# Optimization experiments

Hardware: AMD Instinct MI355X
Metric: run time of the kernel (lower is better)

The kernel has to match this reference:

```python
import jax, jax.numpy as jnp
import numpy as np

B, T, N, D = 4, 12, 512, 128
L = 4            # max_lag + 1 lag encoders
H = D // 2       # lag-encoder hidden dim
THRESHOLD = 0.1


def setup_inputs() -> dict:
    key = jax.random.key(0)
    ks = jax.random.split(key, 10)
    s = 0.02
    return {
        "x":   jax.random.normal(ks[0], (B, T, N, D), dtype=jnp.float32),
        # lag encoders: Linear(D->H), ReLU, Linear(H->D), stacked over L lags
        "W1":  s * jax.random.normal(ks[1], (L, D, H), dtype=jnp.float32),
        "b1":  jnp.zeros((L, H), dtype=jnp.float32),
        "W2":  s * jax.random.normal(ks[2], (L, H, D), dtype=jnp.float32),
        "b2":  jnp.zeros((L, D), dtype=jnp.float32),
        # causal scorer: Linear(2D->D), ReLU, (Dropout=id in eval), Linear(D->1), Sigmoid
        "Ws1": s * jax.random.normal(ks[3], (2 * D, D), dtype=jnp.float32),
        "bs1": jnp.zeros((D,), dtype=jnp.float32),
        "Ws2": s * jax.random.normal(ks[4], (D, 1), dtype=jnp.float32),
        "bs2": jnp.zeros((1,), dtype=jnp.float32),
    }


def reference(x, W1, b1, W2, b2, Ws1, bs1, Ws2, bs2):
    Tdim = x.shape[1]
    # lagged slices x[:, T-1-lag] for lag in 0..L-1 (all lags active since T > max_lag)
    lags = jnp.stack([x[:, max(0, Tdim - 1 - l)] for l in range(L)], axis=1)  # (B,L,N,D)
    h = jax.nn.relu(jnp.einsum('blnd,ldh->blnh', lags, W1) + b1[None, :, None, :])
    enc = jnp.einsum('blnh,lhd->blnd', h, W2) + b2[None, :, None, :]          # (B,L,N,D)
    agg = enc.mean(axis=1)                                                    # (B,N,D)

    # pairwise causal scorer. cat([src, tgt]) @ Ws1 == src @ Ws1[:D] + tgt @ Ws1[D:],
    # avoiding the explicit (B,N,N,2D) concat.
    src_proj = jnp.einsum('bnd,dk->bnk', agg, Ws1[:D])   # (B,N,D)
    tgt_proj = jnp.einsum('bnd,dk->bnk', agg, Ws1[D:])   # (B,N,D)
    pre = src_proj[:, :, None, :] + tgt_proj[:, None, :, :] + bs1  # (B,N,N,D)
    score = jax.nn.sigmoid(jnp.einsum('bijd,d->bij', jax.nn.relu(pre), Ws2[:, 0]) + bs2[0])

    # threshold sparsification + remove self loops
    adj = jnp.where(score > THRESHOLD, score, 0.0)
    adj = adj * (1.0 - jnp.eye(N, dtype=adj.dtype))

    # multi-hop propagation and global max normalization per batch element
    a2 = jnp.matmul(adj, adj)
    a3 = jnp.matmul(a2, adj)
    enhanced = adj + 0.5 * a2 + 0.25 * a3
    mx = jnp.max(enhanced, axis=(-1, -2), keepdims=True)
    return enhanced / (mx + 1e-8)
```

## Files before the change

### kernel.cpp

```cpp
#include <hip/hip_runtime.h>
#include <math.h>

#define Bn 4
#define Tn 12
#define Nn 512
#define Dn 128
#define Ln 4
#define Hn 64

typedef __attribute__((ext_vector_type(8))) short short8;
typedef __attribute__((ext_vector_type(4))) float f32x4;
typedef _Float16 h2 __attribute__((ext_vector_type(2)));

__device__ __forceinline__ unsigned short f2bf(float f) {
    unsigned int u = __float_as_uint(f);
    unsigned int r = (u + 0x7FFF + ((u >> 16) & 1)) >> 16;
    return (unsigned short)r;
}
__device__ __forceinline__ float bf2f(unsigned short s) {
    return __uint_as_float(((unsigned int)s) << 16);
}
__device__ __forceinline__ float fdot2(h2 a, h2 b, float c) {
#if defined(__has_builtin)
#if __has_builtin(__builtin_amdgcn_fdot2)
    return __builtin_amdgcn_fdot2(a, b, c, false);
#else
    return c + (float)a.x*(float)b.x + (float)a.y*(float)b.y;
#endif
#else
    return c + (float)a.x*(float)b.x + (float)a.y*(float)b.y;
#endif
}

__global__ __launch_bounds__(256) void k_prep(
    const float* __restrict__ W1, const float* __restrict__ W2, const float* __restrict__ Ws1,
    unsigned short* __restrict__ w1p, unsigned short* __restrict__ w2p,
    unsigned short* __restrict__ wsp)
{
    int g = blockIdx.x*256 + threadIdx.x;
    unsigned short tmp[8];
    if (g < 4096) {
        int lag = g >> 10, r = g & 1023;
        int n = r >> 4, k8 = r & 15;
        #pragma unroll
        for (int j = 0; j < 8; ++j) tmp[j] = f2bf(W1[(size_t)(lag*128 + k8*8 + j)*64 + n]);
        *(short8*)(w1p + (size_t)lag*8192 + n*128 + k8*8) = *(const short8*)tmp;
    } else if (g < 8192) {
        int r = g - 4096;
        int n = r >> 5, k8 = r & 31;
        #pragma unroll
        for (int j = 0; j < 8; ++j) tmp[j] = f2bf(W2[(size_t)(k8*8 + j)*128 + n]);
        *(short8*)(w2p + (size_t)n*256 + k8*8) = *(const short8*)tmp;
    } else {
        int r = g - 8192;
        int tgt = r >> 11, r2 = r & 2047;
        int n = r2 >> 4, k8 = r2 & 15;
        #pragma unroll
        for (int j = 0; j < 8; ++j) tmp[j] = f2bf(Ws1[(size_t)(tgt*128 + k8*8 + j)*128 + n]);
        *(short8*)(wsp + (size_t)tgt*16384 + n*128 + k8*8) = *(const short8*)tmp;
    }
}

__global__ __launch_bounds__(256) void k_enc(
    const float* __restrict__ x,  const float* __restrict__ b1,
    const float* __restrict__ b2, const float* __restrict__ bs1,
    const unsigned short* __restrict__ w1p, const unsigned short* __restrict__ w2p,
    const unsigned short* __restrict__ wsp,
    unsigned short* __restrict__ spb, unsigned short* __restrict__ tpb,
    unsigned int* __restrict__ maxslot)
{
    __shared__ __align__(16) unsigned short hA[16*264];
    __shared__ __align__(16) unsigned short xA[16*136];
    __shared__ __align__(16) unsigned short aggA[16*136];
    int tid  = threadIdx.x;
    int bid  = blockIdx.x;
    int wv   = __builtin_amdgcn_readfirstlane(tid >> 6);
    int lane = tid & 63;
    if (bid == 0 && tid < Bn) maxslot[tid] = 0u;

    int r0 = bid * 16;
    int bb = r0 >> 9, n0 = r0 & 511;
    int m = lane & 15, q = lane >> 4;
    int colL = lane & 15, rq = lane >> 4;

    for (int lag = 0; lag < Ln; ++lag) {
        __syncthreads();
        {
            const float4* xs = (const float4*)(x + ((size_t)(bb*Tn + (Tn-1-lag))*Nn + n0)*Dn);
            for (int v = tid; v < 512; v += 256) {
                float4 f = xs[v];
                int row = v >> 5, c4 = v & 31;
                ushort4 o = { f2bf(f.x), f2bf(f.y), f2bf(f.z), f2bf(f.w) };
                *(ushort4*)&xA[row*136 + c4*4] = o;
            }
        }
        __syncthreads();
        f32x4 acc = {0.f,0.f,0.f,0.f};
        #pragma unroll
        for (int ks = 0; ks < 4; ++ks) {
            short8 af = *(const short8*)&xA[m*136 + ks*32 + q*8];
            short8 bg = *(const short8*)(w1p + (size_t)lag*8192 + (wv*16+m)*128 + ks*32 + q*8);
            acc = __builtin_amdgcn_mfma_f32_16x16x32_bf16(af, bg, acc, 0, 0, 0);
        }
        int ncol = wv*16 + colL;
        float bv = b1[lag*Hn + ncol];
        #pragma unroll
        for (int reg = 0; reg < 4; ++reg)
            hA[(rq*4+reg)*264 + lag*64 + ncol] = f2bf(fmaxf(acc[reg] + bv, 0.f));
    }
    __syncthreads();

    #pragma unroll
    for (int ch = 0; ch < 2; ++ch) {
        f32x4 acc = {0.f,0.f,0.f,0.f};
        #pragma unroll
        for (int ks = 0; ks < 8; ++ks) {
            short8 af = *(const short8*)&hA[m*264 + ks*32 + q*8];
            short8 bg = *(const short8*)(w2p + (size_t)(ch*64 + wv*16 + m)*256 + ks*32 + q*8);
            acc = __builtin_amdgcn_mfma_f32_16x16x32_bf16(af, bg, acc, 0, 0, 0);
        }
        int col = ch*64 + wv*16 + colL;
        float b2s = b2[col] + b2[Dn+col] + b2[2*Dn+col] + b2[3*Dn+col];
        #pragma unroll
        for (int reg = 0; reg < 4; ++reg)
            aggA[(rq*4+reg)*136 + col] = f2bf(0.25f*(acc[reg] + b2s));
    }
    __syncthreads();

    #pragma unroll
    for (int tgt = 0; tgt < 2; ++tgt) {
        f32x4 acc[2] = {{0.f,0.f,0.f,0.f},{0.f,0.f,0.f,0.f}};
        #pragma unroll
        for (int ks = 0; ks < 4; ++ks) {
            short8 af = *(const short8*)&aggA[m*136 + ks*32 + q*8];
            #pragma unroll
            for (int nt = 0; nt < 2; ++nt) {
                short8 bg = *(const short8*)(wsp + (size_t)tgt*16384 + (wv*32 + nt*16 + m)*128 + ks*32 + q*8);
                acc[nt] = __builtin_amdgcn_mfma_f32_16x16x32_bf16(af, bg, acc[nt], 0, 0, 0);
            }
        }
        unsigned short* dst = tgt ? tpb : spb;
        #pragma unroll
        for (int nt = 0; nt < 2; ++nt) {
            int n = wv*32 + nt*16 + colL;
            float bv = tgt ? 0.f : bs1[n];
            #pragma unroll
            for (int reg = 0; reg < 4; ++reg) {
                _Float16 hv = (_Float16)(acc[nt][reg] + bv);
                dst[(size_t)(r0 + rq*4 + reg)*Dn + n] = __builtin_bit_cast(unsigned short, hv);
            }
        }
    }
}

__global__ __launch_bounds__(256) void k_score(
    const unsigned short* __restrict__ spb, const unsigned short* __restrict__ tpb,
    const float* __restrict__ Ws2, const float* __restrict__ bs2,
    unsigned short* __restrict__ adj_b, unsigned short* __restrict__ adj_bt)
{
    __shared__ unsigned int spl[64*65];
    __shared__ unsigned int tpl[64*65];
    __shared__ unsigned int wl[64];
    int tid = threadIdx.x;
    int wv = __builtin_amdgcn_readfirstlane(tid >> 6);
    int lane = tid & 63;
    int bz = blockIdx.z;
    int i0b = blockIdx.y * 64, j0b = blockIdx.x * 64;
    const unsigned short* spr = spb + (size_t)bz*Nn*Dn;
    const unsigned short* tpr = tpb + (size_t)bz*Nn*Dn;

    for (int v = tid; v < 1024; v += 256) {
        int row = v >> 4, c = v & 15;
        uint4 gs = *(const uint4*)(spr + (size_t)(i0b+row)*Dn + c*8);
        uint4 gt = *(const uint4*)(tpr + (size_t)(j0b+row)*Dn + c*8);
        spl[row*65 + c*4 + 0] = gs.x; spl[row*65 + c*4 + 1] = gs.y;
        spl[row*65 + c*4 + 2] = gs.z; spl[row*65 + c*4 + 3] = gs.w;
        tpl[row*65 + c*4 + 0] = gt.x; tpl[row*65 + c*4 + 1] = gt.y;
        tpl[row*65 + c*4 + 2] = gt.z; tpl[row*65 + c*4 + 3] = gt.w;
    }
    if (tid < 64) {
        h2 hw = { (_Float16)Ws2[tid*2], (_Float16)Ws2[tid*2+1] };
        wl[tid] = __builtin_bit_cast(unsigned int, hw);
    }
    __syncthreads();

    int iq = lane >> 4, jq = lane & 15;
    int iw = wv*16 + iq*4;
    float acc[4][4] = {};
    #pragma unroll 4
    for (int c = 0; c < 64; ++c) {
        h2 wp = __builtin_bit_cast(h2, wl[c]);
        h2 sh[4], th[4];
        #pragma unroll
        for (int ii = 0; ii < 4; ++ii) sh[ii] = __builtin_bit_cast(h2, spl[(iw+ii)*65 + c]);
        #pragma unroll
        for (int jj = 0; jj < 4; ++jj) th[jj] = __builtin_bit_cast(h2, tpl[(jq*4+jj)*65 + c]);
        #pragma unroll
        for (int ii = 0; ii < 4; ++ii)
            #pragma unroll
            for (int jj = 0; jj < 4; ++jj) {
                h2 r = __builtin_elementwise_max(sh[ii] + th[jj], (h2){(_Float16)0.f,(_Float16)0.f});
                acc[ii][jj] = fdot2(r, wp, acc[ii][jj]);
            }
    }
    float bsv = bs2[0];
    int i0 = i0b + iw;
    int j0 = j0b + jq*4;
    float vals[4][4];
    #pragma unroll
    for (int ii = 0; ii < 4; ++ii) {
        int i = i0 + ii;
        #pragma unroll
        for (int jj = 0; jj < 4; ++jj) {
            float z = acc[ii][jj] + bsv;
            float sc = 1.f/(1.f + __expf(-z));
            int j = j0 + jj;
            vals[ii][jj] = (sc > 0.1f && i != j) ? sc : 0.f;
        }
    }
    size_t base = (size_t)bz << 18;
    #pragma unroll
    for (int ii = 0; ii < 4; ++ii) {
        ushort4 rv = make_ushort4(f2bf(vals[ii][0]), f2bf(vals[ii][1]),
                                  f2bf(vals[ii][2]), f2bf(vals[ii][3]));
        *(ushort4*)(adj_b + base + (size_t)(i0+ii)*Nn + j0) = rv;
    }
    #pragma unroll
    for (int jj = 0; jj < 4; ++jj) {
        ushort4 cv = make_ushort4(f2bf(vals[0][jj]), f2bf(vals[1][jj]),
                                  f2bf(vals[2][jj]), f2bf(vals[3][jj]));
        *(ushort4*)(adj_bt + base + (size_t)(j0+jj)*Nn + i0) = cv;
    }
}

__global__ __launch_bounds__(512) void k_prop(
    const unsigned short* __restrict__ adj_b, const unsigned short* __restrict__ adj_bt,
    float* __restrict__ out, unsigned int* __restrict__ maxslot)
{
    __shared__ __align__(16) unsigned short adjA[16*520];
    __shared__ __align__(16) unsigned short a2ls[16*520];
    __shared__ float red[8];
    int tid = threadIdx.x;
    int wv = __builtin_amdgcn_readfirstlane(tid >> 6);
    int lane = tid & 63;
    int i0 = blockIdx.x * 16, bz = blockIdx.y;
    size_t base = (size_t)bz << 18;
    const unsigned short* Ab = adj_b + base;
    const unsigned short* Bb = adj_bt + base;

    for (int v = tid; v < 1024; v += 512) {
        int row = v >> 6, c = v & 63;
        *(short8*)&adjA[row*520 + c*8] = *(const short8*)(Ab + (size_t)(i0+row)*Nn + c*8);
    }
    __syncthreads();

    int m = lane & 15, q = lane >> 4;
    int colL = m, rq = q;
    const unsigned short* Bw = Bb + (size_t)(wv*64 + m)*Nn + q*8;

    f32x4 acc[4];
    short8 bgbuf[4][4];
    #pragma unroll
    for (int pk = 0; pk < 4; ++pk)
        #pragma unroll
        for (int jt = 0; jt < 4; ++jt)
            bgbuf[pk][jt] = *(const short8*)(Bw + jt*16*Nn + pk*32);
    #pragma unroll
    for (int jt = 0; jt < 4; ++jt) acc[jt] = (f32x4){0.f,0.f,0.f,0.f};
    #pragma unroll
    for (int ks = 0; ks < 16; ++ks) {
        short8 af = *(const short8*)&adjA[m*520 + ks*32 + q*8];
        short8 cur[4];
        #pragma unroll
        for (int jt = 0; jt < 4; ++jt) cur[jt] = bgbuf[ks & 3][jt];
        if (ks < 12) {
            #pragma unroll
            for (int jt = 0; jt < 4; ++jt)
                bgbuf[ks & 3][jt] = *(const short8*)(Bw + jt*16*Nn + (ks+4)*32);
        }
        #pragma unroll
        for (int jt = 0; jt < 4; ++jt)
            acc[jt] = __builtin_amdgcn_mfma_f32_16x16x32_bf16(af, cur[jt], acc[jt], 0, 0, 0);
    }
    #pragma unroll
    for (int jt = 0; jt < 4; ++jt) {
        int j = wv*64 + jt*16 + colL;
        #pragma unroll
        for (int reg = 0; reg < 4; ++reg)
            a2ls[(rq*4+reg)*520 + j] = f2bf(acc[jt][reg]);
    }
    __syncthreads();

    #pragma unroll
    for (int pk = 0; pk < 4; ++pk)
        #pragma unroll
        for (int jt = 0; jt < 4; ++jt)
            bgbuf[pk][jt] = *(const short8*)(Bw + jt*16*Nn + pk*32);
    #pragma unroll
    for (int jt = 0; jt < 4; ++jt) acc[jt] = (f32x4){0.f,0.f,0.f,0.f};
    #pragma unroll
    for (int ks = 0; ks < 16; ++ks) {
        short8 af = *(const short8*)&a2ls[m*520 + ks*32 + q*8];
        short8 cur[4];
        #pragma unroll
        for (int jt = 0; jt < 4; ++jt) cur[jt] = bgbuf[ks & 3][jt];
        if (ks < 12) {
            #pragma unroll
            for (int jt = 0; jt < 4; ++jt)
                bgbuf[ks & 3][jt] = *(const short8*)(Bw + jt*16*Nn + (ks+4)*32);
        }
        #pragma unroll
        for (int jt = 0; jt < 4; ++jt)
            acc[jt] = __builtin_amdgcn_mfma_f32_16x16x32_bf16(af, cur[jt], acc[jt], 0, 0, 0);
    }

    float lmax = 0.f;
    #pragma unroll
    for (int jt = 0; jt < 4; ++jt) {
        int j = wv*64 + jt*16 + colL;
        #pragma unroll
        for (int reg = 0; reg < 4; ++reg) {
            int r = rq*4 + reg;
            float e = bf2f(adjA[r*520 + j]) + 0.5f*bf2f(a2ls[r*520 + j]) + 0.25f*acc[jt][reg];
            out[base + (size_t)(i0+r)*Nn + j] = e;
            lmax = fmaxf(lmax, e);
        }
    }
    #pragma unroll
    for (int s = 1; s < 64; s <<= 1) lmax = fmaxf(lmax, __shfl_xor(lmax, s, 64));
    if (lane == 0) red[wv] = lmax;
    __syncthreads();
    if (tid == 0) {
        float mx = red[0];
        #pragma unroll
        for (int w = 1; w < 8; ++w) mx = fmaxf(mx, red[w]);
        atomicMax(maxslot + bz, __float_as_uint(mx));
    }
}

__global__ __launch_bounds__(256) void k_norm(float* __restrict__ out,
                                              const unsigned int* __restrict__ maxslot)
{
    int idx = blockIdx.x*256 + threadIdx.x;
    int b = idx >> 16;
    float m = __uint_as_float(maxslot[b]);
    float inv = 1.f/(m + 1e-8f);
    float4* p = (float4*)out + idx;
    float4 v = *p;
    v.x *= inv; v.y *= inv; v.z *= inv; v.w *= inv;
    *p = v;
}

extern "C" void kernel_launch(void* const* d_in, const int* in_sizes, int n_in,
                              void* d_out, int out_size, void* d_ws, size_t ws_size,
                              hipStream_t stream) {
    const float* x   = (const float*)d_in[0];
    const float* W1  = (const float*)d_in[1];
    const float* b1  = (const float*)d_in[2];
    const float* W2  = (const float*)d_in[3];
    const float* b2  = (const float*)d_in[4];
    const float* Ws1 = (const float*)d_in[5];
    const float* bs1 = (const float*)d_in[6];
    const float* Ws2 = (const float*)d_in[7];
    const float* bs2 = (const float*)d_in[8];
    float* out = (float*)d_out;

    unsigned char* wsb = (unsigned char*)d_ws;
    unsigned short* spb    = (unsigned short*)(wsb);
    unsigned short* tpb    = (unsigned short*)(wsb + (512u<<10));
    unsigned short* adj_b  = (unsigned short*)(wsb + (1024u<<10));
    unsigned short* adj_bt = (unsigned short*)(wsb + (3072u<<10));
    unsigned int*   maxslot= (unsigned int*)(wsb + (7168u<<10));
    unsigned short* w1p    = (unsigned short*)(wsb + (7172u<<10));
    unsigned short* w2p    = (unsigned short*)(wsb + (7236u<<10));
    unsigned short* wsp    = (unsigned short*)(wsb + (7300u<<10));

    k_prep <<<dim3(48),       256, 0, stream>>>(W1, W2, Ws1, w1p, w2p, wsp);
    k_enc  <<<dim3(128),      256, 0, stream>>>(x, b1, b2, bs1, w1p, w2p, wsp, spb, tpb, maxslot);
    k_score<<<dim3(8, 8, Bn), 256, 0, stream>>>(spb, tpb, Ws2, bs2, adj_b, adj_bt);
    k_prop <<<dim3(32, Bn),   512, 0, stream>>>(adj_b, adj_bt, out, maxslot);
    k_norm <<<dim3(1024),     256, 0, stream>>>(out, maxslot);
}
```

Measured before the change: 132.7 us.

## Pre-pack transposed adjacency into MFMA fragment order and widen encoder blocks

k_score now writes the transposed adjacency in a layout packed to MFMA B-fragment order, so each lane in k_prop does a contiguous 16-byte load with the wave fully coalesced instead of strided row reads. k_enc goes to 512 threads, loads all four lag slices at once and splits lags and output halves across waves, which removes the per-lag barrier loop. The LDS row padding in k_prop changes from 520 to 514. The packing arithmetic adds index math to k_score's stores, and the new padding may change LDS bank-conflict behaviour.

```diff
diff --git a/kernel.cpp b/kernel.cpp
--- a/kernel.cpp
+++ b/kernel.cpp
@@ -61,7 +61,7 @@
     }
 }
 
-__global__ __launch_bounds__(256) void k_enc(
+__global__ __launch_bounds__(512) void k_enc(
     const float* __restrict__ x,  const float* __restrict__ b1,
     const float* __restrict__ b2, const float* __restrict__ bs1,
     const unsigned short* __restrict__ w1p, const unsigned short* __restrict__ w2p,
@@ -69,8 +69,8 @@
     unsigned short* __restrict__ spb, unsigned short* __restrict__ tpb,
     unsigned int* __restrict__ maxslot)
 {
+    __shared__ __align__(16) unsigned short xAll[4][16*136];
     __shared__ __align__(16) unsigned short hA[16*264];
-    __shared__ __align__(16) unsigned short xA[16*136];
     __shared__ __align__(16) unsigned short aggA[16*136];
     int tid  = threadIdx.x;
     int bid  = blockIdx.x;
@@ -83,43 +83,48 @@
     int m = lane & 15, q = lane >> 4;
     int colL = lane & 15, rq = lane >> 4;
 
-    for (int lag = 0; lag < Ln; ++lag) {
-        __syncthreads();
-        {
-            const float4* xs = (const float4*)(x + ((size_t)(bb*Tn + (Tn-1-lag))*Nn + n0)*Dn);
-            for (int v = tid; v < 512; v += 256) {
-                float4 f = xs[v];
-                int row = v >> 5, c4 = v & 31;
-                ushort4 o = { f2bf(f.x), f2bf(f.y), f2bf(f.z), f2bf(f.w) };
-                *(ushort4*)&xA[row*136 + c4*4] = o;
+    for (int v = tid; v < 2048; v += 512) {
+        int lag = v >> 9, r = v & 511;
+        int row = r >> 5, c4 = r & 31;
+        const float4* xs = (const float4*)(x + ((size_t)(bb*Tn + (Tn-1-lag))*Nn + n0)*Dn);
+        float4 f = xs[row*32 + c4];
+        ushort4 o = { f2bf(f.x), f2bf(f.y), f2bf(f.z), f2bf(f.w) };
+        *(ushort4*)&xAll[lag][row*136 + c4*4] = o;
+    }
+    __syncthreads();
+
+    {
+        int lag = wv >> 1, hf = wv & 1;
+        f32x4 acc[2] = {{0.f,0.f,0.f,0.f},{0.f,0.f,0.f,0.f}};
+        #pragma unroll
+        for (int ks = 0; ks < 4; ++ks) {
+            short8 af = *(const short8*)&xAll[lag][m*136 + ks*32 + q*8];
+            #pragma unroll
+            for (int nt = 0; nt < 2; ++nt) {
+                short8 bg = *(const short8*)(w1p + (size_t)lag*8192 + (hf*32 + nt*16 + m)*128 + ks*32 + q*8);
+                acc[nt] = __builtin_amdgcn_mfma_f32_16x16x32_bf16(af, bg, acc[nt], 0, 0, 0);
             }
         }
-        __syncthreads();
-        f32x4 acc = {0.f,0.f,0.f,0.f};
-        #pragma unroll
-        for (int ks = 0; ks < 4; ++ks) {
-            short8 af = *(const short8*)&xA[m*136 + ks*32 + q*8];
-            short8 bg = *(const short8*)(w1p + (size_t)lag*8192 + (wv*16+m)*128 + ks*32 + q*8);
-            acc = __builtin_amdgcn_mfma_f32_16x16x32_bf16(af, bg, acc, 0, 0, 0);
-        }
-        int ncol = wv*16 + colL;
-        float bv = b1[lag*Hn + ncol];
-        #pragma unroll
-        for (int reg = 0; reg < 4; ++reg)
-            hA[(rq*4+reg)*264 + lag*64 + ncol] = f2bf(fmaxf(acc[reg] + bv, 0.f));
-    }
-    __syncthreads();
-
-    #pragma unroll
-    for (int ch = 0; ch < 2; ++ch) {
+        #pragma unroll
+        for (int nt = 0; nt < 2; ++nt) {
+            int ncol = hf*32 + nt*16 + colL;
+            float bv = b1[lag*Hn + ncol];
+            #pragma unroll
+            for (int reg = 0; reg < 4; ++reg)
+                hA[(rq*4+reg)*264 + lag*64 + ncol] = f2bf(fmaxf(acc[nt][reg] + bv, 0.f));
+        }
+    }
+    __syncthreads();
+
+    {
         f32x4 acc = {0.f,0.f,0.f,0.f};
         #pragma unroll
         for (int ks = 0; ks < 8; ++ks) {
             short8 af = *(const short8*)&hA[m*264 + ks*32 + q*8];
-            short8 bg = *(const short8*)(w2p + (size_t)(ch*64 + wv*16 + m)*256 + ks*32 + q*8);
+            short8 bg = *(const short8*)(w2p + (size_t)(wv*16 + m)*256 + ks*32 + q*8);
             acc = __builtin_amdgcn_mfma_f32_16x16x32_bf16(af, bg, acc, 0, 0, 0);
         }
-        int col = ch*64 + wv*16 + colL;
+        int col = wv*16 + colL;
         float b2s = b2[col] + b2[Dn+col] + b2[2*Dn+col] + b2[3*Dn+col];
         #pragma unroll
         for (int reg = 0; reg < 4; ++reg)
@@ -127,22 +132,22 @@
     }
     __syncthreads();
 
-    #pragma unroll
-    for (int tgt = 0; tgt < 2; ++tgt) {
+    {
+        int tgt = wv >> 2, wv4 = wv & 3;
         f32x4 acc[2] = {{0.f,0.f,0.f,0.f},{0.f,0.f,0.f,0.f}};
         #pragma unroll
         for (int ks = 0; ks < 4; ++ks) {
             short8 af = *(const short8*)&aggA[m*136 + ks*32 + q*8];
             #pragma unroll
             for (int nt = 0; nt < 2; ++nt) {
-                short8 bg = *(const short8*)(wsp + (size_t)tgt*16384 + (wv*32 + nt*16 + m)*128 + ks*32 + q*8);
+                short8 bg = *(const short8*)(wsp + (size_t)tgt*16384 + (wv4*32 + nt*16 + m)*128 + ks*32 + q*8);
                 acc[nt] = __builtin_amdgcn_mfma_f32_16x16x32_bf16(af, bg, acc[nt], 0, 0, 0);
             }
         }
         unsigned short* dst = tgt ? tpb : spb;
         #pragma unroll
         for (int nt = 0; nt < 2; ++nt) {
-            int n = wv*32 + nt*16 + colL;
+            int n = wv4*32 + nt*16 + colL;
             float bv = tgt ? 0.f : bs1[n];
             #pragma unroll
             for (int reg = 0; reg < 4; ++reg) {
@@ -156,7 +161,7 @@
 __global__ __launch_bounds__(256) void k_score(
     const unsigned short* __restrict__ spb, const unsigned short* __restrict__ tpb,
     const float* __restrict__ Ws2, const float* __restrict__ bs2,
-    unsigned short* __restrict__ adj_b, unsigned short* __restrict__ adj_bt)
+    unsigned short* __restrict__ adj_b, unsigned short* __restrict__ adj_pk)
 {
     __shared__ unsigned int spl[64*65];
     __shared__ unsigned int tpl[64*65];
@@ -225,103 +230,106 @@
                                   f2bf(vals[ii][2]), f2bf(vals[ii][3]));
         *(ushort4*)(adj_b + base + (size_t)(i0+ii)*Nn + j0) = rv;
     }
+    int kblk = i0 >> 5, qq = (i0 >> 3) & 3, t0 = i0 & 7;
     #pragma unroll
     for (int jj = 0; jj < 4; ++jj) {
+        int j = j0 + jj;
+        int jt = j >> 4, mm = j & 15;
         ushort4 cv = make_ushort4(f2bf(vals[0][jj]), f2bf(vals[1][jj]),
                                   f2bf(vals[2][jj]), f2bf(vals[3][jj]));
-        *(ushort4*)(adj_bt + base + (size_t)(j0+jj)*Nn + i0) = cv;
+        *(ushort4*)(adj_pk + base + (size_t)(kblk*32 + jt)*512 + (qq*16 + mm)*8 + t0) = cv;
     }
 }
 
 __global__ __launch_bounds__(512) void k_prop(
-    const unsigned short* __restrict__ adj_b, const unsigned short* __restrict__ adj_bt,
+    const unsigned short* __restrict__ adj_b, const unsigned short* __restrict__ adj_pk,
     float* __restrict__ out, unsigned int* __restrict__ maxslot)
 {
-    __shared__ __align__(16) unsigned short adjA[16*520];
-    __shared__ __align__(16) unsigned short a2ls[16*520];
+    __shared__ __align__(16) unsigned short adjA[16*514];
+    __shared__ __align__(16) unsigned short a2ls[16*514];
     __shared__ float red[8];
     int tid = threadIdx.x;
     int wv = __builtin_amdgcn_readfirstlane(tid >> 6);
     int lane = tid & 63;
     int i0 = blockIdx.x * 16, bz = blockIdx.y;
     size_t base = (size_t)bz << 18;
-    const unsigned short* Ab = adj_b + base;
-    const unsigned short* Bb = adj_bt + base;
 
     for (int v = tid; v < 1024; v += 512) {
-        int row = v >> 6, c = v & 63;
-        *(short8*)&adjA[row*520 + c*8] = *(const short8*)(Ab + (size_t)(i0+row)*Nn + c*8);
+        int row = v >> 6, c8 = v & 63;
+        *(short8*)&adjA[row*514 + c8*8] =
+            *(const short8*)(adj_b + base + (size_t)(i0+row)*Nn + c8*8);
     }
     __syncthreads();
 
     int m = lane & 15, q = lane >> 4;
     int colL = m, rq = q;
-    const unsigned short* Bw = Bb + (size_t)(wv*64 + m)*Nn + q*8;
+    const unsigned short* pkw = adj_pk + base + (size_t)(wv*4)*512 + lane*8;
 
     f32x4 acc[4];
-    short8 bgbuf[4][4];
-    #pragma unroll
-    for (int pk = 0; pk < 4; ++pk)
-        #pragma unroll
-        for (int jt = 0; jt < 4; ++jt)
-            bgbuf[pk][jt] = *(const short8*)(Bw + jt*16*Nn + pk*32);
-    #pragma unroll
-    for (int jt = 0; jt < 4; ++jt) acc[jt] = (f32x4){0.f,0.f,0.f,0.f};
-    #pragma unroll
-    for (int ks = 0; ks < 16; ++ks) {
-        short8 af = *(const short8*)&adjA[m*520 + ks*32 + q*8];
+    short8 ring[4][4];
+
+    #pragma unroll
+    for (int pb = 0; pb < 4; ++pb)
+        #pragma unroll
+        for (int nt = 0; nt < 4; ++nt)
+            ring[pb][nt] = *(const short8*)(pkw + (size_t)pb*16384 + nt*512);
+    #pragma unroll
+    for (int nt = 0; nt < 4; ++nt) acc[nt] = (f32x4){0.f,0.f,0.f,0.f};
+    #pragma unroll
+    for (int kb = 0; kb < 16; ++kb) {
+        short8 af = *(const short8*)&adjA[m*514 + kb*32 + q*8];
         short8 cur[4];
         #pragma unroll
-        for (int jt = 0; jt < 4; ++jt) cur[jt] = bgbuf[ks & 3][jt];
-        if (ks < 12) {
-            #pragma unroll
-            for (int jt = 0; jt < 4; ++jt)
-                bgbuf[ks & 3][jt] = *(const short8*)(Bw + jt*16*Nn + (ks+4)*32);
-        }
-        #pragma unroll
-        for (int jt = 0; jt < 4; ++jt)
-            acc[jt] = __builtin_amdgcn_mfma_f32_16x16x32_bf16(af, cur[jt], acc[jt], 0, 0, 0);
-    }
-    #pragma unroll
-    for (int jt = 0; jt < 4; ++jt) {
-        int j = wv*64 + jt*16 + colL;
+        for (int nt = 0; nt < 4; ++nt) cur[nt] = ring[kb & 3][nt];
+        if (kb < 12) {
+            #pragma unroll
+            for (int nt = 0; nt < 4; ++nt)
+                ring[kb & 3][nt] = *(const short8*)(pkw + (size_t)(kb+4)*16384 + nt*512);
+        }
+        #pragma unroll
+        for (int nt = 0; nt < 4; ++nt)
+            acc[nt] = __builtin_amdgcn_mfma_f32_16x16x32_bf16(af, cur[nt], acc[nt], 0, 0, 0);
+    }
+    #pragma unroll
+    for (int nt = 0; nt < 4; ++nt) {
+        int j = wv*64 + nt*16 + colL;
         #pragma unroll
         for (int reg = 0; reg < 4; ++reg)
-            a2ls[(rq*4+reg)*520 + j] = f2bf(acc[jt][reg]);
-    }
-    __syncthreads();
-
-    #pragma unroll
-    for (int pk = 0; pk < 4; ++pk)
-        #pragma unroll
-        for (int jt = 0; jt < 4; ++jt)
-            bgbuf[pk][jt] = *(const short8*)(Bw + jt*16*Nn + pk*32);
-    #pragma unroll
-    for (int jt = 0; jt < 4; ++jt) acc[jt] = (f32x4){0.f,0.f,0.f,0.f};
-    #pragma unroll
-    for (int ks = 0; ks < 16; ++ks) {
-        short8 af = *(const short8*)&a2ls[m*520 + ks*32 + q*8];
+            a2ls[(rq*4+reg)*514 + j] = f2bf(acc[nt][reg]);
+    }
+    __syncthreads();
+
+    #pragma unroll
+    for (int pb = 0; pb < 4; ++pb)
+        #pragma unroll
+        for (int nt = 0; nt < 4; ++nt)
+            ring[pb][nt] = *(const short8*)(pkw + (size_t)pb*16384 + nt*512);
+    #pragma unroll
+    for (int nt = 0; nt < 4; ++nt) acc[nt] = (f32x4){0.f,0.f,0.f,0.f};
+    #pragma unroll
+    for (int kb = 0; kb < 16; ++kb) {
+        short8 af = *(const short8*)&a2ls[m*514 + kb*32 + q*8];
         short8 cur[4];
         #pragma unroll
-        for (int jt = 0; jt < 4; ++jt) cur[jt] = bgbuf[ks & 3][jt];
-        if (ks < 12) {
-            #pragma unroll
-            for (int jt = 0; jt < 4; ++jt)
-                bgbuf[ks & 3][jt] = *(const short8*)(Bw + jt*16*Nn + (ks+4)*32);
-        }
-        #pragma unroll
-        for (int jt = 0; jt < 4; ++jt)
-            acc[jt] = __builtin_amdgcn_mfma_f32_16x16x32_bf16(af, cur[jt], acc[jt], 0, 0, 0);
+        for (int nt = 0; nt < 4; ++nt) cur[nt] = ring[kb & 3][nt];
+        if (kb < 12) {
+            #pragma unroll
+            for (int nt = 0; nt < 4; ++nt)
+                ring[kb & 3][nt] = *(const short8*)(pkw + (size_t)(kb+4)*16384 + nt*512);
+        }
+        #pragma unroll
+        for (int nt = 0; nt < 4; ++nt)
+            acc[nt] = __builtin_amdgcn_mfma_f32_16x16x32_bf16(af, cur[nt], acc[nt], 0, 0, 0);
     }
 
     float lmax = 0.f;
     #pragma unroll
-    for (int jt = 0; jt < 4; ++jt) {
-        int j = wv*64 + jt*16 + colL;
+    for (int nt = 0; nt < 4; ++nt) {
+        int j = wv*64 + nt*16 + colL;
         #pragma unroll
         for (int reg = 0; reg < 4; ++reg) {
             int r = rq*4 + reg;
-            float e = bf2f(adjA[r*520 + j]) + 0.5f*bf2f(a2ls[r*520 + j]) + 0.25f*acc[jt][reg];
+            float e = bf2f(adjA[r*514 + j]) + 0.5f*bf2f(a2ls[r*514 + j]) + 0.25f*acc[nt][reg];
             out[base + (size_t)(i0+r)*Nn + j] = e;
             lmax = fmaxf(lmax, e);
         }
@@ -369,15 +377,15 @@
     unsigned short* spb    = (unsigned short*)(wsb);
     unsigned short* tpb    = (unsigned short*)(wsb + (512u<<10));
     unsigned short* adj_b  = (unsigned short*)(wsb + (1024u<<10));
-    unsigned short* adj_bt = (unsigned short*)(wsb + (3072u<<10));
+    unsigned short* adj_pk = (unsigned short*)(wsb + (3072u<<10));
     unsigned int*   maxslot= (unsigned int*)(wsb + (7168u<<10));
     unsigned short* w1p    = (unsigned short*)(wsb + (7172u<<10));
     unsigned short* w2p    = (unsigned short*)(wsb + (7236u<<10));
     unsigned short* wsp    = (unsigned short*)(wsb + (7300u<<10));
 
     k_prep <<<dim3(48),       256, 0, stream>>>(W1, W2, Ws1, w1p, w2p, wsp);
-    k_enc  <<<dim3(128),      256, 0, stream>>>(x, b1, b2, bs1, w1p, w2p, wsp, spb, tpb, maxslot);
-    k_score<<<dim3(8, 8, Bn), 256, 0, stream>>>(spb, tpb, Ws2, bs2, adj_b, adj_bt);
-    k_prop <<<dim3(32, Bn),   512, 0, stream>>>(adj_b, adj_bt, out, maxslot);
+    k_enc  <<<dim3(128),      512, 0, stream>>>(x, b1, b2, bs1, w1p, w2p, wsp, spb, tpb, maxslot);
+    k_score<<<dim3(8, 8, Bn), 256, 0, stream>>>(spb, tpb, Ws2, bs2, adj_b, adj_pk);
+    k_prop <<<dim3(32, Bn),   512, 0, stream>>>(adj_b, adj_pk, out, maxslot);
     k_norm <<<dim3(1024),     256, 0, stream>>>(out, maxslot);
 }
```

After: 122.6 us. 7.7% less time.
